# Kernel optimization log

Hardware: AMD Instinct MI355X
Metric: run time of the kernel (lower is better)

## Reference

```python
import jax, jax.numpy as jnp
import numpy as np

NUM_NODES = 50000
NUM_EDGES = 800000
INPUT_DIM = 256
OUTPUT_DIM = 256
NUM_HEADS = 8
HEAD_DIM = OUTPUT_DIM // NUM_HEADS


def setup_inputs() -> dict:
    key = jax.random.key(0)
    ks = jax.random.split(key, 14)
    x = jax.random.normal(ks[0], (NUM_NODES, INPUT_DIM), dtype=jnp.float32)
    edge_index = jax.random.randint(ks[1], (2, NUM_EDGES), 0, NUM_NODES, dtype=jnp.int32)
    # timestamps in seconds over ~11.5 days so log1p(|dt|/3600) is informative
    edge_time = jax.random.uniform(ks[2], (NUM_EDGES,), dtype=jnp.float32) * 1e6
    node_time = jax.random.uniform(ks[3], (NUM_NODES,), dtype=jnp.float32) * 1e6
    s_in = 1.0 / np.sqrt(INPUT_DIM)
    s_out = 1.0 / np.sqrt(OUTPUT_DIM)
    s_t = 1.0 / np.sqrt(2.0)
    Wq = jax.random.uniform(ks[4], (INPUT_DIM, OUTPUT_DIM), jnp.float32, -s_in, s_in)
    bq = jax.random.uniform(ks[5], (OUTPUT_DIM,), jnp.float32, -s_in, s_in)
    Wk = jax.random.uniform(ks[6], (INPUT_DIM, OUTPUT_DIM), jnp.float32, -s_in, s_in)
    bk = jax.random.uniform(ks[7], (OUTPUT_DIM,), jnp.float32, -s_in, s_in)
    Wv = jax.random.uniform(ks[8], (INPUT_DIM, OUTPUT_DIM), jnp.float32, -s_in, s_in)
    bv = jax.random.uniform(ks[9], (OUTPUT_DIM,), jnp.float32, -s_in, s_in)
    Wt = jax.random.uniform(ks[10], (2, NUM_HEADS), jnp.float32, -s_t, s_t)
    bt = jax.random.uniform(ks[11], (NUM_HEADS,), jnp.float32, -s_t, s_t)
    Wo = jax.random.uniform(ks[12], (OUTPUT_DIM, OUTPUT_DIM), jnp.float32, -s_out, s_out)
    bo = jax.random.uniform(ks[13], (OUTPUT_DIM,), jnp.float32, -s_out, s_out)
    return {"x": x, "edge_index": edge_index, "edge_time": edge_time, "node_time": node_time,
            "Wq": Wq, "bq": bq, "Wk": Wk, "bk": bk, "Wv": Wv, "bv": bv,
            "Wt": Wt, "bt": bt, "Wo": Wo, "bo": bo}


def reference(x, edge_index, edge_time, node_time, Wq, bq, Wk, bk, Wv, bv, Wt, bt, Wo, bo):
    n = x.shape[0]
    q = (x @ Wq + bq).reshape(n, NUM_HEADS, HEAD_DIM)
    k = (x @ Wk + bk).reshape(n, NUM_HEADS, HEAD_DIM)
    v = (x @ Wv + bv).reshape(n, NUM_HEADS, HEAD_DIM)
    src, dst = edge_index[0], edge_index[1]
    # temporal features per edge
    time_diff = edge_time - node_time[dst]
    time_features = jnp.stack(
        [jnp.sign(time_diff), jnp.log1p(jnp.abs(time_diff) / 3600.0)], axis=-1)  # [E, 2]
    temporal_weights = time_features @ Wt + bt  # [E, H]
    scale = HEAD_DIM ** -0.5
    scores = jnp.einsum('ehd,ehd->eh', q[dst], k[src]) * scale + temporal_weights  # [E, H]
    # softmax over ALL edges per head (dim=0), as in the original
    alpha = jax.nn.softmax(scores, axis=0)  # [E, H]
    msg = alpha[..., None] * v[src]  # [E, H, D]
    out = jax.ops.segment_sum(msg, dst, num_segments=n)  # [N, H, D]
    out = out.reshape(n, OUTPUT_DIM)
    return out @ Wo + bo
```

## Files before the change

### kernel.cpp

```cpp
#include <hip/hip_runtime.h>
#include <hip/hip_bf16.h>

#define NUM_NODES 50000
#define NUM_EDGES 800000
#define NUM_HEADS 8
#define HEAD_DIM 32
#define SCAN_BLOCKS 49
#define NCHUNK32 1563

typedef unsigned short ushort8 __attribute__((ext_vector_type(8)));
typedef float f32x4 __attribute__((ext_vector_type(4)));
typedef __bf16 bf16x8 __attribute__((ext_vector_type(8)));
typedef _Float16 h2 __attribute__((ext_vector_type(2)));

union BF8 { ushort8 u; bf16x8 b; };
union H8 { ushort8 u; h2 h[4]; };

#if defined(__has_builtin)
#if __has_builtin(__builtin_amdgcn_fdot2)
#define FDOT2(a, b, c) __builtin_amdgcn_fdot2((a), (b), (c), false)
#endif
#endif
#ifndef FDOT2
#define FDOT2(a, b, c) ((float)(a)[0] * (float)(b)[0] + (float)(a)[1] * (float)(b)[1] + (c))
#endif

__device__ __forceinline__ unsigned float_to_key(float f) {
    int i = __float_as_int(f);
    return (i >= 0) ? ((unsigned)i | 0x80000000u) : ~(unsigned)i;
}
__device__ __forceinline__ float key_to_float(unsigned u) {
    unsigned b = (u & 0x80000000u) ? (u & 0x7fffffffu) : ~u;
    return __int_as_float((int)b);
}
__device__ __forceinline__ float bf2f(unsigned short u) {
    return __uint_as_float(((unsigned)u) << 16);
}
__device__ __forceinline__ unsigned short f2bf(float f) {
    unsigned u = __float_as_uint(f);
    unsigned r = (u + 0x7fffu + ((u >> 16) & 1u)) >> 16;
    return (unsigned short)r;
}
__device__ __forceinline__ unsigned short f2h(float f) {
    _Float16 h = (_Float16)f;
    return *(unsigned short*)&h;
}
__device__ __forceinline__ float h2f(unsigned short u) {
    _Float16 h = *(const _Float16*)&u;
    return (float)h;
}

__global__ __launch_bounds__(256) void deg_kernel(const int* __restrict__ dst_idx, int* __restrict__ deg) {
    int e = blockIdx.x * 256 + threadIdx.x;
    if (e < NUM_EDGES) atomicAdd(&deg[dst_idx[e]], 1);
}

__global__ __launch_bounds__(1024) void scanA_kernel(
    const int* __restrict__ deg, int* __restrict__ offs, int* __restrict__ blocksum)
{
    __shared__ int buf[1024];
    int tid = threadIdx.x;
    int i = blockIdx.x * 1024 + tid;
    int v = (i < NUM_NODES) ? deg[i] : 0;
    buf[tid] = v;
    __syncthreads();
    for (int off = 1; off < 1024; off <<= 1) {
        int t = (tid >= off) ? buf[tid - off] : 0;
        __syncthreads();
        buf[tid] += t;
        __syncthreads();
    }
    if (i < NUM_NODES) offs[i] = buf[tid] - v;
    if (tid == 1023) blocksum[blockIdx.x] = buf[1023];
}

__global__ __launch_bounds__(64) void scanB_kernel(
    const int* __restrict__ blocksum, int* __restrict__ carry, int* __restrict__ offs)
{
    if (threadIdx.x == 0) {
        int acc = 0;
        for (int b = 0; b < SCAN_BLOCKS; b++) { carry[b] = acc; acc += blocksum[b]; }
        offs[NUM_NODES] = acc;
    }
}

__global__ __launch_bounds__(256) void scanC_kernel(
    int* __restrict__ offs, const int* __restrict__ carry, int* __restrict__ cursor)
{
    int i = blockIdx.x * 256 + threadIdx.x;
    if (i < NUM_NODES) {
        int v = offs[i] + carry[i >> 10];
        offs[i] = v;
        cursor[i] = v;
    }
}

__global__ __launch_bounds__(256) void fillA_kernel(
    const int* __restrict__ dst_idx, int* __restrict__ cursor, int* __restrict__ edge_of)
{
    int e = blockIdx.x * 256 + threadIdx.x;
    if (e < NUM_EDGES) {
        int pos = atomicAdd(&cursor[dst_idx[e]], 1);
        edge_of[pos] = e;
    }
}

__global__ __launch_bounds__(256) void fillB_kernel(
    const int* __restrict__ edge_of,
    const int* __restrict__ src_idx, const int* __restrict__ dst_idx,
    const float* __restrict__ edge_time, const float* __restrict__ node_time,
    int2* __restrict__ sd, unsigned* __restrict__ tfh)
{
    int pos = blockIdx.x * 256 + threadIdx.x;
    if (pos < NUM_EDGES) {
        int e = edge_of[pos];
        int s = src_idx[e];
        int d = dst_idx[e];
        int2 v; v.x = s; v.y = d;
        sd[pos] = v;
        float td = edge_time[e] - node_time[d];
        float t0 = (td > 0.f) ? 1.f : ((td < 0.f) ? -1.f : 0.f);
        float t1 = log1pf(fabsf(td) * (1.f / 3600.f));
        tfh[pos] = (unsigned)f2h(t0) | ((unsigned)f2h(t1) << 16);
    }
}

__global__ __launch_bounds__(256) void wtrans_kernel(
    const float* __restrict__ Wq, const float* __restrict__ Wk,
    const float* __restrict__ Wv, const float* __restrict__ Wo,
    unsigned short* __restrict__ Wt)
{
    __shared__ float t[64][65];
    int nb = blockIdx.x * 64;
    int kb = blockIdx.y * 64;
    int g = nb >> 8;
    const float* W = (g == 0) ? Wq : (g == 1) ? Wk : (g == 2) ? Wv : Wo;
    int n0 = nb & 255;
    int tx = threadIdx.x & 63;
    int ty = threadIdx.x >> 6;
#pragma unroll
    for (int i = 0; i < 16; i++) {
        int k = i * 4 + ty;
        t[tx][k] = W[(size_t)(kb + k) * 256 + n0 + tx];
    }
    __syncthreads();
#pragma unroll
    for (int i = 0; i < 16; i++) {
        int n = i * 4 + ty;
        Wt[(size_t)(nb + n) * 256 + kb + tx] = f2bf(t[n][tx]);
    }
}

__global__ __launch_bounds__(256) void wpack_kernel(
    const unsigned short* __restrict__ Wt, unsigned short* __restrict__ Wpk)
{
    int gid = blockIdx.x * 256 + threadIdx.x;
    int lane = gid & 63;
    int fragidx = gid >> 6;
    int c2 = fragidx & 7;
    int nf = (fragidx >> 3) & 3;
    int cb = (fragidx >> 5) & 3;
    int g = fragidx >> 7;
    int l16 = lane & 15;
    int kg = lane >> 4;
    int n_col = g * 256 + cb * 64 + nf * 16 + l16;
    int k0 = c2 * 32 + kg * 8;
    ushort8 v = *(const ushort8*)(Wt + (size_t)n_col * 256 + k0);
    *(ushort8*)(Wpk + (size_t)gid * 8) = v;
}

__global__ __launch_bounds__(256) void gemm_qkv_mfma7(
    const float* __restrict__ A, int M,
    const unsigned short* __restrict__ Wpk,
    const float* __restrict__ b0, const float* __restrict__ b1, const float* __restrict__ b2,
    unsigned short* __restrict__ O0, unsigned short* __restrict__ O1, unsigned short* __restrict__ O2)
{
    __shared__ unsigned short As[64 * 256];
    int tid = threadIdx.x;
    int rowbase = blockIdx.x * 64;

    {
        int rsub = tid >> 6;
        int c4 = (tid & 63) * 4;
        int cchunk = (tid & 63) >> 1;
        int sub = (tid & 1);
#pragma unroll
        for (int it = 0; it < 16; it++) {
            int row = it * 4 + rsub;
            int grow = rowbase + row;
            float4 av = make_float4(0.f, 0.f, 0.f, 0.f);
            if (grow < M) av = *(const float4*)(A + (size_t)grow * 256 + c4);
            ushort4 o;
            o.x = f2bf(av.x); o.y = f2bf(av.y); o.z = f2bf(av.z); o.w = f2bf(av.w);
            unsigned byte = row * 512 + ((unsigned)(cchunk ^ (row & 7)) << 4) + sub * 8;
            *(ushort4*)((char*)As + byte) = o;
        }
    }
    __syncthreads();

    int lane = tid & 63;
    int wid = tid >> 6;
    int l16 = lane & 15;
    int kg = lane >> 4;

#pragma unroll
    for (int p = 0; p < 3; p++) {
        const float* bias = (p == 0) ? b0 : (p == 1) ? b1 : b2;
        unsigned short* O = (p == 0) ? O0 : (p == 1) ? O1 : O2;

        f32x4 acc[4][4];
#pragma unroll
        for (int m = 0; m < 4; m++)
#pragma unroll
            for (int n = 0; n < 4; n++) acc[m][n] = (f32x4)(0.0f);

        const ushort8* wbase = (const ushort8*)(Wpk + ((size_t)(p * 4 + wid) * 2048 + lane) * 8);

#pragma unroll
        for (int c2 = 0; c2 < 8; c2++) {
            bf16x8 wfr[4];
#pragma unroll
            for (int n = 0; n < 4; n++) {
                BF8 t; t.u = wbase[(n * 8 + c2) * 64];
                wfr[n] = t.b;
            }
            bf16x8 afr[4];
#pragma unroll
            for (int m = 0; m < 4; m++) {
                int row = m * 16 + l16;
                int cchunk = (c2 * 4 + kg) ^ (row & 7);
                BF8 t;
                t.u = *(const ushort8*)((const char*)As + row * 512 + (cchunk << 4));
                afr[m] = t.b;
            }
#pragma unroll
            for (int m = 0; m < 4; m++)
#pragma unroll
                for (int n = 0; n < 4; n++)
                    acc[m][n] = __builtin_amdgcn_mfma_f32_16x16x32_bf16(wfr[n], afr[m], acc[m][n], 0, 0, 0);
        }

#pragma unroll
        for (int m = 0; m < 4; m++) {
            int node = rowbase + m * 16 + l16;
            if (node >= M) continue;
#pragma unroll
            for (int n = 0; n < 4; n++) {
                int lc = wid * 64 + n * 16 + kg * 4;
                float4 bv = *(const float4*)(bias + lc);
                ushort4 o;
                if (p < 2) {
                    o.x = f2h(acc[m][n][0] + bv.x);
                    o.y = f2h(acc[m][n][1] + bv.y);
                    o.z = f2h(acc[m][n][2] + bv.z);
                    o.w = f2h(acc[m][n][3] + bv.w);
                } else {
                    o.x = f2bf(acc[m][n][0] + bv.x);
                    o.y = f2bf(acc[m][n][1] + bv.y);
                    o.z = f2bf(acc[m][n][2] + bv.z);
                    o.w = f2bf(acc[m][n][3] + bv.w);
                }
                int hh = lc >> 5, dd = lc & 31;
                *(ushort4*)(O + ((size_t)hh * NUM_NODES + node) * 32 + dd) = o;
            }
        }
    }
}

__global__ __launch_bounds__(256) void gemm_out_mfma6(
    const unsigned short* __restrict__ aggb, int M,
    const unsigned short* __restrict__ Wpk,
    const float* __restrict__ bias, const float* __restrict__ kscale,
    float* __restrict__ C)
{
    __shared__ unsigned short As[64 * 256];
    int tid = threadIdx.x;
    int rowbase = blockIdx.x * 64;

    {
        int rsub = tid >> 6;
        int c4 = (tid & 63) * 4;
        int cchunk = (tid & 63) >> 1;
        int sub = (tid & 1);
        int hh = c4 >> 5, dd = c4 & 31;
        float ks = kscale[hh];
#pragma unroll
        for (int it = 0; it < 16; it++) {
            int row = it * 4 + rsub;
            int grow = rowbase + row;
            ushort4 av = make_ushort4(0, 0, 0, 0);
            if (grow < M) av = *(const ushort4*)(aggb + ((size_t)hh * NUM_NODES + grow) * 32 + dd);
            ushort4 o;
            o.x = f2bf(bf2f(av.x) * ks); o.y = f2bf(bf2f(av.y) * ks);
            o.z = f2bf(bf2f(av.z) * ks); o.w = f2bf(bf2f(av.w) * ks);
            unsigned byte = row * 512 + ((unsigned)(cchunk ^ (row & 7)) << 4) + sub * 8;
            *(ushort4*)((char*)As + byte) = o;
        }
    }
    __syncthreads();

    int lane = tid & 63;
    int wid = tid >> 6;
    int l16 = lane & 15;
    int kg = lane >> 4;

    f32x4 acc[4][4];
#pragma unroll
    for (int m = 0; m < 4; m++)
#pragma unroll
        for (int n = 0; n < 4; n++) acc[m][n] = (f32x4)(0.0f);

    const ushort8* wbase = (const ushort8*)(Wpk + ((size_t)wid * 2048 + lane) * 8);

#pragma unroll
    for (int c2 = 0; c2 < 8; c2++) {
        bf16x8 wfr[4];
#pragma unroll
        for (int n = 0; n < 4; n++) {
            BF8 t; t.u = wbase[(n * 8 + c2) * 64];
            wfr[n] = t.b;
        }
        bf16x8 afr[4];
#pragma unroll
        for (int m = 0; m < 4; m++) {
            int row = m * 16 + l16;
            int cchunk = (c2 * 4 + kg) ^ (row & 7);
            BF8 t;
            t.u = *(const ushort8*)((const char*)As + row * 512 + (cchunk << 4));
            afr[m] = t.b;
        }
#pragma unroll
        for (int m = 0; m < 4; m++)
#pragma unroll
            for (int n = 0; n < 4; n++)
                acc[m][n] = __builtin_amdgcn_mfma_f32_16x16x32_bf16(wfr[n], afr[m], acc[m][n], 0, 0, 0);
    }

#pragma unroll
    for (int m = 0; m < 4; m++) {
        int node = rowbase + m * 16 + l16;
        if (node >= M) continue;
#pragma unroll
        for (int n = 0; n < 4; n++) {
            int col = wid * 64 + n * 16 + kg * 4;
            float4 bv = *(const float4*)(bias + col);
            float4 o;
            o.x = acc[m][n][0] + bv.x;
            o.y = acc[m][n][1] + bv.y;
            o.z = acc[m][n][2] + bv.z;
            o.w = acc[m][n][3] + bv.w;
            *(float4*)(C + (size_t)node * 256 + col) = o;
        }
    }
}

__global__ __launch_bounds__(256) void score5_kernel(
    const unsigned short* __restrict__ qh, const unsigned short* __restrict__ kh,
    const int2* __restrict__ sd, const unsigned* __restrict__ tfh,
    const float* __restrict__ Wt, const float* __restrict__ bt,
    float* __restrict__ scores, unsigned* __restrict__ partialmax)
{
    __shared__ unsigned sm;
    int tid = threadIdx.x;
    if (tid == 0) sm = 0u;
    __syncthreads();
    int h = blockIdx.x & 7;
    int blk = blockIdx.x >> 3;
    float wt0 = Wt[h], wt1 = Wt[8 + h], btv = bt[h];
    const unsigned short* qhh = qh + (size_t)h * NUM_NODES * 32;
    const unsigned short* khh = kh + (size_t)h * NUM_NODES * 32;
    float* sc_h = scores + (size_t)h * NUM_EDGES;
    unsigned mykey = 0u;
    const int stride = 256 * 256;
    for (int pos = blk * 256 + tid; pos < NUM_EDGES; pos += stride) {
        int2 e = sd[pos];
        unsigned tp = tfh[pos];
        float t0 = h2f((unsigned short)(tp & 0xffffu));
        float t1 = h2f((unsigned short)(tp >> 16));
        const ushort8* qp = (const ushort8*)(qhh + (size_t)e.y * 32);
        const ushort8* kp = (const ushort8*)(khh + (size_t)e.x * 32);
        float dotv = 0.f;
#pragma unroll
        for (int i = 0; i < 4; i++) {
            H8 a, b;
            a.u = qp[i]; b.u = kp[i];
#pragma unroll
            for (int j = 0; j < 4; j++) dotv = FDOT2(a.h[j], b.h[j], dotv);
        }
        float sc = dotv * 0.17677669529663687f + (t0 * wt0 + t1 * wt1 + btv);
        sc_h[pos] = sc;
        unsigned kkey = float_to_key(sc);
        mykey = (kkey > mykey) ? kkey : mykey;
    }
#pragma unroll
    for (int off = 32; off > 0; off >>= 1) {
        unsigned o = __shfl_xor(mykey, off, 64);
        mykey = (o > mykey) ? o : mykey;
    }
    if ((tid & 63) == 0) atomicMax(&sm, mykey);
    __syncthreads();
    if (tid == 0) partialmax[blockIdx.x] = sm;
}

__global__ __launch_bounds__(256) void reduce_max3_kernel(
    const unsigned* __restrict__ partialmax, float* __restrict__ headmax)
{
    int tid = threadIdx.x;
    int h = tid >> 5, lane = tid & 31;
    unsigned m = 0u;
    for (int i = lane; i < 256; i += 32) {
        unsigned v = partialmax[i * 8 + h];
        m = (v > m) ? v : m;
    }
    for (int off = 16; off > 0; off >>= 1) {
        unsigned o = __shfl_down(m, off, 32);
        m = (o > m) ? o : m;
    }
    if (lane == 0) headmax[h] = key_to_float(m);
}

__global__ __launch_bounds__(256) void aggregate8_kernel(
    const unsigned short* __restrict__ vh, const float* __restrict__ scores,
    const int2* __restrict__ sd, const int* __restrict__ offs,
    const float* __restrict__ headmax, unsigned short* __restrict__ aggb,
    float* __restrict__ psum_part)
{
    __shared__ int sSrc[512];
    __shared__ float sP[512];
    __shared__ float blocksum;
    int tid = threadIdx.x;
    int h = blockIdx.x & 7;
    int chunk = blockIdx.x >> 3;
    int nodebase = chunk * 32;
    int g = tid >> 3;
    int ln = tid & 7;
    int node = nodebase + g;
    float m = headmax[h];
    const float* sc_h = scores + (size_t)h * NUM_EDGES;
    const unsigned short* vhh = vh + (size_t)h * NUM_NODES * 32;
    if (tid == 0) blocksum = 0.f;

    int blkstart = offs[nodebase];
    int blkend = offs[(nodebase + 32 < NUM_NODES) ? (nodebase + 32) : NUM_NODES];
    int start = 0, end = 0;
    if (node < NUM_NODES) { start = offs[node]; end = offs[node + 1]; }

    f32x4 a0 = (f32x4)(0.f), a1 = (f32x4)(0.f);
    float ps = 0.f;

    for (int t0 = blkstart; t0 < blkend; t0 += 512) {
        int cnt = min(512, blkend - t0);
        __syncthreads();
        for (int i = tid; i < cnt; i += 256) {
            sSrc[i] = sd[t0 + i].x;
            float p = __expf(sc_h[t0 + i] - m);
            sP[i] = p;
            ps += p;
        }
        __syncthreads();
        int lo = (start > t0) ? start : t0;
        int hi = (end < t0 + cnt) ? end : (t0 + cnt);
        int cb = lo;
        for (; cb + 2 <= hi; cb += 2) {
            int i0 = cb - t0;
            int s0 = sSrc[i0], s1 = sSrc[i0 + 1];
            float p0 = sP[i0], p1 = sP[i0 + 1];
            ushort4 v0 = *(const ushort4*)(vhh + (size_t)s0 * 32 + ln * 4);
            ushort4 v1 = *(const ushort4*)(vhh + (size_t)s1 * 32 + ln * 4);
            a0[0] += p0 * bf2f(v0.x); a0[1] += p0 * bf2f(v0.y);
            a0[2] += p0 * bf2f(v0.z); a0[3] += p0 * bf2f(v0.w);
            a1[0] += p1 * bf2f(v1.x); a1[1] += p1 * bf2f(v1.y);
            a1[2] += p1 * bf2f(v1.z); a1[3] += p1 * bf2f(v1.w);
        }
        if (cb < hi) {
            int i0 = cb - t0;
            int s0 = sSrc[i0];
            float p0 = sP[i0];
            ushort4 v0 = *(const ushort4*)(vhh + (size_t)s0 * 32 + ln * 4);
            a0[0] += p0 * bf2f(v0.x); a0[1] += p0 * bf2f(v0.y);
            a0[2] += p0 * bf2f(v0.z); a0[3] += p0 * bf2f(v0.w);
        }
    }

    if (node < NUM_NODES) {
        ushort4 o;
        o.x = f2bf(a0[0] + a1[0]); o.y = f2bf(a0[1] + a1[1]);
        o.z = f2bf(a0[2] + a1[2]); o.w = f2bf(a0[3] + a1[3]);
        *(ushort4*)(aggb + ((size_t)h * NUM_NODES + node) * 32 + ln * 4) = o;
    }

    __syncthreads();
#pragma unroll
    for (int off = 32; off > 0; off >>= 1) ps += __shfl_xor(ps, off, 64);
    if ((tid & 63) == 0) atomicAdd(&blocksum, ps);
    __syncthreads();
    if (tid == 0) psum_part[blockIdx.x] = blocksum;
}

__global__ __launch_bounds__(256) void reduce_psum2_kernel(
    const float* __restrict__ psum_part, float* __restrict__ headinv)
{
    int tid = threadIdx.x;
    int h = tid >> 5, lane = tid & 31;
    float s = 0.f;
    for (int i = lane; i < NCHUNK32; i += 32) s += psum_part[i * 8 + h];
    for (int off = 16; off > 0; off >>= 1) s += __shfl_down(s, off, 32);
    if (lane == 0) headinv[h] = 1.f / s;
}

extern "C" void kernel_launch(void* const* d_in, const int* in_sizes, int n_in,
                              void* d_out, int out_size, void* d_ws, size_t ws_size,
                              hipStream_t stream) {
    const float* x = (const float*)d_in[0];
    const int* ei = (const int*)d_in[1];
    const int* src_idx = ei;
    const int* dst_idx = ei + NUM_EDGES;
    const float* edge_time = (const float*)d_in[2];
    const float* node_time = (const float*)d_in[3];
    const float* Wq = (const float*)d_in[4];  const float* bq = (const float*)d_in[5];
    const float* Wk = (const float*)d_in[6];  const float* bk = (const float*)d_in[7];
    const float* Wv = (const float*)d_in[8];  const float* bv = (const float*)d_in[9];
    const float* Wt = (const float*)d_in[10]; const float* bt = (const float*)d_in[11];
    const float* Wo = (const float*)d_in[12]; const float* bo = (const float*)d_in[13];
    float* out = (float*)d_out;

    char* w = (char*)d_ws;
    unsigned short* qb = (unsigned short*)w; w += (size_t)NUM_NODES * 256 * 2;
    unsigned short* kb = (unsigned short*)w; w += (size_t)NUM_NODES * 256 * 2;
    unsigned short* vb = (unsigned short*)w; w += (size_t)NUM_NODES * 256 * 2;
    float* scores = (float*)w;      w += (size_t)NUM_EDGES * 8 * 4;
    unsigned short* aggb = (unsigned short*)w; w += (size_t)NUM_NODES * 256 * 2;
    int2* sd = (int2*)w;            w += (size_t)NUM_EDGES * 8;
    unsigned* tfh = (unsigned*)w;   w += (size_t)NUM_EDGES * 4;
    int* edge_of = (int*)w;         w += (size_t)NUM_EDGES * 4;
    int* deg = (int*)w;             w += (size_t)NUM_NODES * 4;
    int* offs = (int*)w;            w += (size_t)(NUM_NODES + 1) * 4;
    int* cursor = (int*)w;          w += (size_t)NUM_NODES * 4;
    unsigned* partialmax = (unsigned*)w; w += 2048 * 4;
    float* psum_part = (float*)w;   w += (size_t)NCHUNK32 * 8 * 4;
    float* headmax = (float*)w;     w += 8 * 4;
    float* headinv = (float*)w;     w += 8 * 4;
    int* blocksum = (int*)w;        w += 64 * 4;
    int* bcarry = (int*)w;          w += 64 * 4;
    unsigned short* Wtb = (unsigned short*)w; w += (size_t)1024 * 256 * 2;
    unsigned short* Wpk = (unsigned short*)w; w += (size_t)1024 * 256 * 2;

    hipMemsetAsync(deg, 0, (size_t)NUM_NODES * 4, stream);

    dim3 gw(16, 4);
    wtrans_kernel<<<gw, 256, 0, stream>>>(Wq, Wk, Wv, Wo, Wtb);
    wpack_kernel<<<128, 256, 0, stream>>>(Wtb, Wpk);

    deg_kernel<<<(NUM_EDGES + 255) / 256, 256, 0, stream>>>(dst_idx, deg);
    scanA_kernel<<<SCAN_BLOCKS, 1024, 0, stream>>>(deg, offs, blocksum);
    scanB_kernel<<<1, 64, 0, stream>>>(blocksum, bcarry, offs);
    scanC_kernel<<<(NUM_NODES + 255) / 256, 256, 0, stream>>>(offs, bcarry, cursor);
    fillA_kernel<<<(NUM_EDGES + 255) / 256, 256, 0, stream>>>(dst_idx, cursor, edge_of);
    fillB_kernel<<<(NUM_EDGES + 255) / 256, 256, 0, stream>>>(
        edge_of, src_idx, dst_idx, edge_time, node_time, sd, tfh);

    gemm_qkv_mfma7<<<(NUM_NODES + 63) / 64, 256, 0, stream>>>(
        x, NUM_NODES, Wpk, bq, bk, bv, qb, kb, vb);

    score5_kernel<<<2048, 256, 0, stream>>>(qb, kb, sd, tfh, Wt, bt, scores, partialmax);
    reduce_max3_kernel<<<1, 256, 0, stream>>>(partialmax, headmax);

    aggregate8_kernel<<<NCHUNK32 * 8, 256, 0, stream>>>(
        vb, scores, sd, offs, headmax, aggb, psum_part);
    reduce_psum2_kernel<<<1, 256, 0, stream>>>(psum_part, headinv);

    gemm_out_mfma6<<<(NUM_NODES + 63) / 64, 256, 0, stream>>>(
        aggb, NUM_NODES, Wpk + (size_t)768 * 256, bo, headinv, out);
}
```

Measured before the change: 369.3 us.

## Pack edge indices to 16-bit, store scores in fp16, precompute temporal weights

Source and destination indices are packed into one 32-bit word, which works because the node count fits in 16 bits. Scores are stored as fp16 instead of fp32. The per-head temporal weight is computed once in fillB and stored as fp16, instead of being rebuilt from time features in the score kernel. Nontemporal loads and stores are used on the streaming edge arrays. The aim is to cut the bytes moved through the edge-parallel score and aggregate passes. The cost is lower score precision, which can perturb the softmax, plus extra writes of per-head temporal weights in fillB.

```diff
diff --git a/kernel.cpp b/kernel.cpp
--- a/kernel.cpp
+++ b/kernel.cpp
@@ -109,19 +109,23 @@
     const int* __restrict__ edge_of,
     const int* __restrict__ src_idx, const int* __restrict__ dst_idx,
     const float* __restrict__ edge_time, const float* __restrict__ node_time,
-    int2* __restrict__ sd, unsigned* __restrict__ tfh)
+    const float* __restrict__ Wt, const float* __restrict__ bt,
+    unsigned* __restrict__ sdp, unsigned short* __restrict__ twh)
 {
     int pos = blockIdx.x * 256 + threadIdx.x;
     if (pos < NUM_EDGES) {
-        int e = edge_of[pos];
+        int e = __builtin_nontemporal_load(&edge_of[pos]);
         int s = src_idx[e];
         int d = dst_idx[e];
-        int2 v; v.x = s; v.y = d;
-        sd[pos] = v;
+        __builtin_nontemporal_store((unsigned)s | ((unsigned)d << 16), &sdp[pos]);
         float td = edge_time[e] - node_time[d];
         float t0 = (td > 0.f) ? 1.f : ((td < 0.f) ? -1.f : 0.f);
         float t1 = log1pf(fabsf(td) * (1.f / 3600.f));
-        tfh[pos] = (unsigned)f2h(t0) | ((unsigned)f2h(t1) << 16);
+#pragma unroll
+        for (int h = 0; h < 8; h++) {
+            float tw = t0 * Wt[h] + t1 * Wt[8 + h] + bt[h];
+            __builtin_nontemporal_store(f2h(tw), &twh[(size_t)h * NUM_EDGES + pos]);
+        }
     }
 }
 
@@ -354,11 +358,10 @@
     }
 }
 
-__global__ __launch_bounds__(256) void score5_kernel(
+__global__ __launch_bounds__(256) void score6_kernel(
     const unsigned short* __restrict__ qh, const unsigned short* __restrict__ kh,
-    const int2* __restrict__ sd, const unsigned* __restrict__ tfh,
-    const float* __restrict__ Wt, const float* __restrict__ bt,
-    float* __restrict__ scores, unsigned* __restrict__ partialmax)
+    const unsigned* __restrict__ sdp, const unsigned short* __restrict__ twh,
+    unsigned short* __restrict__ scores, unsigned* __restrict__ partialmax)
 {
     __shared__ unsigned sm;
     int tid = threadIdx.x;
@@ -366,19 +369,19 @@
     __syncthreads();
     int h = blockIdx.x & 7;
     int blk = blockIdx.x >> 3;
-    float wt0 = Wt[h], wt1 = Wt[8 + h], btv = bt[h];
     const unsigned short* qhh = qh + (size_t)h * NUM_NODES * 32;
     const unsigned short* khh = kh + (size_t)h * NUM_NODES * 32;
-    float* sc_h = scores + (size_t)h * NUM_EDGES;
+    const unsigned short* tw_h = twh + (size_t)h * NUM_EDGES;
+    unsigned short* sc_h = scores + (size_t)h * NUM_EDGES;
     unsigned mykey = 0u;
     const int stride = 256 * 256;
     for (int pos = blk * 256 + tid; pos < NUM_EDGES; pos += stride) {
-        int2 e = sd[pos];
-        unsigned tp = tfh[pos];
-        float t0 = h2f((unsigned short)(tp & 0xffffu));
-        float t1 = h2f((unsigned short)(tp >> 16));
-        const ushort8* qp = (const ushort8*)(qhh + (size_t)e.y * 32);
-        const ushort8* kp = (const ushort8*)(khh + (size_t)e.x * 32);
+        unsigned sdv = __builtin_nontemporal_load(&sdp[pos]);
+        int s = sdv & 0xffffu;
+        int d = sdv >> 16;
+        float tw = h2f(__builtin_nontemporal_load(&tw_h[pos]));
+        const ushort8* qp = (const ushort8*)(qhh + (size_t)d * 32);
+        const ushort8* kp = (const ushort8*)(khh + (size_t)s * 32);
         float dotv = 0.f;
 #pragma unroll
         for (int i = 0; i < 4; i++) {
@@ -387,8 +390,8 @@
 #pragma unroll
             for (int j = 0; j < 4; j++) dotv = FDOT2(a.h[j], b.h[j], dotv);
         }
-        float sc = dotv * 0.17677669529663687f + (t0 * wt0 + t1 * wt1 + btv);
-        sc_h[pos] = sc;
+        float sc = dotv * 0.17677669529663687f + tw;
+        __builtin_nontemporal_store(f2h(sc), &sc_h[pos]);
         unsigned kkey = float_to_key(sc);
         mykey = (kkey > mykey) ? kkey : mykey;
     }
@@ -419,9 +422,9 @@
     if (lane == 0) headmax[h] = key_to_float(m);
 }
 
-__global__ __launch_bounds__(256) void aggregate8_kernel(
-    const unsigned short* __restrict__ vh, const float* __restrict__ scores,
-    const int2* __restrict__ sd, const int* __restrict__ offs,
+__global__ __launch_bounds__(256) void aggregate9_kernel(
+    const unsigned short* __restrict__ vh, const unsigned short* __restrict__ scores,
+    const unsigned* __restrict__ sdp, const int* __restrict__ offs,
     const float* __restrict__ headmax, unsigned short* __restrict__ aggb,
     float* __restrict__ psum_part)
 {
@@ -436,7 +439,7 @@
     int ln = tid & 7;
     int node = nodebase + g;
     float m = headmax[h];
-    const float* sc_h = scores + (size_t)h * NUM_EDGES;
+    const unsigned short* sc_h = scores + (size_t)h * NUM_EDGES;
     const unsigned short* vhh = vh + (size_t)h * NUM_NODES * 32;
     if (tid == 0) blocksum = 0.f;
 
@@ -452,8 +455,8 @@
         int cnt = min(512, blkend - t0);
         __syncthreads();
         for (int i = tid; i < cnt; i += 256) {
-            sSrc[i] = sd[t0 + i].x;
-            float p = __expf(sc_h[t0 + i] - m);
+            sSrc[i] = (int)(__builtin_nontemporal_load(&sdp[t0 + i]) & 0xffffu);
+            float p = __expf(h2f(__builtin_nontemporal_load(&sc_h[t0 + i])) - m);
             sP[i] = p;
             ps += p;
         }
@@ -528,10 +531,10 @@
     unsigned short* qb = (unsigned short*)w; w += (size_t)NUM_NODES * 256 * 2;
     unsigned short* kb = (unsigned short*)w; w += (size_t)NUM_NODES * 256 * 2;
     unsigned short* vb = (unsigned short*)w; w += (size_t)NUM_NODES * 256 * 2;
-    float* scores = (float*)w;      w += (size_t)NUM_EDGES * 8 * 4;
+    unsigned short* scores = (unsigned short*)w; w += (size_t)NUM_EDGES * 8 * 2;
+    unsigned short* twh = (unsigned short*)w; w += (size_t)NUM_EDGES * 8 * 2;
     unsigned short* aggb = (unsigned short*)w; w += (size_t)NUM_NODES * 256 * 2;
-    int2* sd = (int2*)w;            w += (size_t)NUM_EDGES * 8;
-    unsigned* tfh = (unsigned*)w;   w += (size_t)NUM_EDGES * 4;
+    unsigned* sdp = (unsigned*)w;   w += (size_t)NUM_EDGES * 4;
     int* edge_of = (int*)w;         w += (size_t)NUM_EDGES * 4;
     int* deg = (int*)w;             w += (size_t)NUM_NODES * 4;
     int* offs = (int*)w;            w += (size_t)(NUM_NODES + 1) * 4;
@@ -557,16 +560,16 @@
     scanC_kernel<<<(NUM_NODES + 255) / 256, 256, 0, stream>>>(offs, bcarry, cursor);
     fillA_kernel<<<(NUM_EDGES + 255) / 256, 256, 0, stream>>>(dst_idx, cursor, edge_of);
     fillB_kernel<<<(NUM_EDGES + 255) / 256, 256, 0, stream>>>(
-        edge_of, src_idx, dst_idx, edge_time, node_time, sd, tfh);
+        edge_of, src_idx, dst_idx, edge_time, node_time, Wt, bt, sdp, twh);
 
     gemm_qkv_mfma7<<<(NUM_NODES + 63) / 64, 256, 0, stream>>>(
         x, NUM_NODES, Wpk, bq, bk, bv, qb, kb, vb);
 
-    score5_kernel<<<2048, 256, 0, stream>>>(qb, kb, sd, tfh, Wt, bt, scores, partialmax);
+    score6_kernel<<<2048, 256, 0, stream>>>(qb, kb, sdp, twh, scores, partialmax);
     reduce_max3_kernel<<<1, 256, 0, stream>>>(partialmax, headmax);
 
-    aggregate8_kernel<<<NCHUNK32 * 8, 256, 0, stream>>>(
-        vb, scores, sd, offs, headmax, aggb, psum_part);
+    aggregate9_kernel<<<NCHUNK32 * 8, 256, 0, stream>>>(
+        vb, scores, sdp, offs, headmax, aggb, psum_part);
     reduce_psum2_kernel<<<1, 256, 0, stream>>>(psum_part, headinv);
 
     gemm_out_mfma6<<<(NUM_NODES + 63) / 64, 256, 0, stream>>>(
```

Measured after the change: 382.9 us. 1.04x slower.
